# Kernel optimization log

Measured on AMD Instinct MI355X. Metric: run time of the kernel, lower is better.

## Reference

```python
import jax, jax.numpy as jnp
import numpy as np


def setup_inputs() -> dict:
    key = jax.random.key(0)
    k1, k2, k3, k4 = jax.random.split(key, 4)
    E, A = 1024, 64
    embedded = jax.random.normal(k1, (4, 4096, E), dtype=jnp.float32)
    # nn.Linear(E, A, bias=False) weight has shape [A, E]; y = x @ W.T
    W_K = jax.random.normal(k2, (A, E), dtype=jnp.float32) * (E ** -0.5)
    W_Q = jax.random.normal(k3, (A, E), dtype=jnp.float32) * (E ** -0.5)
    W_V = jax.random.normal(k4, (A, E), dtype=jnp.float32) * (E ** -0.5)
    return {"embedded": embedded, "W_K": W_K, "W_Q": W_Q, "W_V": W_V}


def reference(embedded, W_K, W_Q, W_V):
    A = W_K.shape[0]
    K = jnp.einsum('bse,ae->bsa', embedded, W_K)
    Q = jnp.einsum('bse,ae->bsa', embedded, W_Q)
    V = jnp.einsum('bse,ae->bsa', embedded, W_V)
    scores = jnp.einsum('bqa,bka->bqk', Q, K) / jnp.sqrt(jnp.float32(A))
    S = K.shape[1]
    causal = jnp.tril(jnp.ones((S, S), dtype=bool))  # True = keep
    scores = jnp.where(causal[None, :, :], scores, -jnp.inf)
    attn = jax.nn.softmax(scores, axis=2)
    out = jnp.einsum('bqk,bka->bqa', attn, V)
    return jnp.round(out, decimals=4)
```

## Files before the change

### kernel.cpp

```cpp
#include <hip/hip_runtime.h>
#include <math.h>

#define B_DIM 4
#define S_DIM 4096
#define E_DIM 1024
#define A_DIM 64
#define M_TOT (B_DIM * S_DIM)

typedef __bf16 v8bf __attribute__((ext_vector_type(8)));
typedef __bf16 v4bf __attribute__((ext_vector_type(4)));
typedef float  v4f  __attribute__((ext_vector_type(4)));

__device__ __forceinline__ v4f mfma16(v8bf a, v8bf b, v4f c) {
    return __builtin_amdgcn_mfma_f32_16x16x32_bf16(a, b, c, 0, 0, 0);
}

__device__ __forceinline__ void lds_dma16(const void* g, void* l) {
    __builtin_amdgcn_global_load_lds(
        (const __attribute__((address_space(1))) unsigned int*)g,
        (__attribute__((address_space(3))) unsigned int*)l, 16, 0, 0);
}

__global__ __launch_bounds__(256) void wconv_kernel(
    const float* __restrict__ Wk, const float* __restrict__ Wq,
    const float* __restrict__ Wv, __bf16* __restrict__ Wb)
{
    const int i = blockIdx.x * 256 + threadIdx.x;
    const int w = i >> 14;
    const int off = (i & 16383) * 4;
    const float* s = ((w == 0) ? Wk : (w == 1) ? Wq : Wv) + off;
    float4 v = *(const float4*)s;
    v4bf o;
    o[0] = (__bf16)v.x; o[1] = (__bf16)v.y; o[2] = (__bf16)v.z; o[3] = (__bf16)v.w;
    *(v4bf*)(Wb + (size_t)w * 65536 + off) = o;
}

__global__ __launch_bounds__(256) void qkv_proj_mfma(
    const float* __restrict__ X,
    const __bf16* __restrict__ Wb,
    __bf16* __restrict__ Kb,
    __bf16* __restrict__ Qb,
    __bf16* __restrict__ Vt)
{
    const int r0   = blockIdx.x * 32;
    const int w    = threadIdx.x >> 6;
    const int lane = threadIdx.x & 63;
    const int L    = lane & 15;
    const int quad = lane >> 4;
    const int cbase = w * 48;

    __shared__ __align__(16) char smem[9216 + 49152];
    __bf16* Xs = (__bf16*)smem;
    __bf16* Bs = (__bf16*)(smem + 9216);
    float (*Tv)[65] = (float(*)[65])smem;

    v4f acc[2][3];
#pragma unroll
    for (int mi = 0; mi < 2; ++mi)
#pragma unroll
        for (int nt = 0; nt < 3; ++nt) acc[mi][nt] = (v4f){0.f, 0.f, 0.f, 0.f};

    const int brow_l  = lane >> 3;
    const int bchunk  = lane & 7;
    const int bgchunk = bchunk ^ brow_l;
    auto stageB = [&](int kc, int buf) {
#pragma unroll
        for (int j = 0; j < 6; ++j) {
            const int rowbase = w * 48 + j * 8;
            const __bf16* g = Wb + (size_t)(rowbase + brow_l) * E_DIM
                              + kc * 64 + bgchunk * 8;
            lds_dma16(g, Bs + buf * 12288 + rowbase * 64);
        }
    };

    const int xrow_i = (lane >> 4);
    const int xcol   = (lane & 15) * 4;
    float4 xr[2];
    auto loadX = [&](int kc) {
#pragma unroll
        for (int i = 0; i < 2; ++i) {
            const int row = i * 16 + w * 4 + xrow_i;
            xr[i] = *(const float4*)(X + (size_t)(r0 + row) * E_DIM + kc * 64 + xcol);
        }
    };
    auto flushX = [&](int buf) {
#pragma unroll
        for (int i = 0; i < 2; ++i) {
            const int row = i * 16 + w * 4 + xrow_i;
            v4bf o;
            o[0] = (__bf16)xr[i].x; o[1] = (__bf16)xr[i].y;
            o[2] = (__bf16)xr[i].z; o[3] = (__bf16)xr[i].w;
            *(v4bf*)(Xs + buf * 2304 + row * 72 + xcol) = o;
        }
    };

    stageB(0, 0);
    loadX(0);
    flushX(0);
    __syncthreads();

#pragma unroll 1
    for (int kc = 0; kc < 16; ++kc) {
        const int cur = kc & 1;
        if (kc < 15) {
            stageB(kc + 1, cur ^ 1);
            loadX(kc + 1);
        }
        v8bf afr[2][2];
#pragma unroll
        for (int mi = 0; mi < 2; ++mi)
#pragma unroll
            for (int ka = 0; ka < 2; ++ka)
                afr[mi][ka] = *(const v8bf*)(Xs + cur * 2304 +
                                (mi * 16 + L) * 72 + ka * 32 + quad * 8);
        v8bf bfr[3][2];
#pragma unroll
        for (int nt = 0; nt < 3; ++nt)
#pragma unroll
            for (int ka = 0; ka < 2; ++ka) {
                const int R = cbase + nt * 16 + L;
                const int slot = (ka * 4 + quad) ^ (R & 7);
                bfr[nt][ka] = *(const v8bf*)(Bs + cur * 12288 + R * 64 + slot * 8);
            }
#pragma unroll
        for (int mi = 0; mi < 2; ++mi)
#pragma unroll
            for (int nt = 0; nt < 3; ++nt)
#pragma unroll
                for (int ka = 0; ka < 2; ++ka)
                    acc[mi][nt] = mfma16(afr[mi][ka], bfr[nt][ka], acc[mi][nt]);

        if (kc < 15) flushX(cur ^ 1);
        __syncthreads();
    }

#pragma unroll
    for (int nt = 0; nt < 3; ++nt) {
        const int c0 = cbase + nt * 16;
        if (c0 < 64) {
#pragma unroll
            for (int mi = 0; mi < 2; ++mi)
#pragma unroll
                for (int r = 0; r < 4; ++r)
                    Kb[(size_t)(r0 + mi * 16 + quad * 4 + r) * A_DIM + c0 + L] =
                        (__bf16)acc[mi][nt][r];
        } else if (c0 < 128) {
#pragma unroll
            for (int mi = 0; mi < 2; ++mi)
#pragma unroll
                for (int r = 0; r < 4; ++r)
                    Qb[(size_t)(r0 + mi * 16 + quad * 4 + r) * A_DIM + (c0 - 64) + L] =
                        (__bf16)(acc[mi][nt][r] * 0.125f);
        } else {
#pragma unroll
            for (int mi = 0; mi < 2; ++mi)
#pragma unroll
                for (int r = 0; r < 4; ++r)
                    Tv[mi * 16 + quad * 4 + r][(c0 - 128) + L] = acc[mi][nt][r];
        }
    }
    __syncthreads();

    {
        const int batch = r0 >> 12;
        const int s0    = r0 & 4095;
        const int a     = threadIdx.x >> 2;
        const int part  = threadIdx.x & 3;
        __bf16* vrow = Vt + (size_t)(batch * 64 + a) * S_DIM + s0 + part * 8;
        v8bf pk;
#pragma unroll
        for (int j = 0; j < 8; ++j)
            pk[j] = (__bf16)Tv[part * 8 + j][a];
        *(v8bf*)vrow = pk;
    }
}

__global__ __launch_bounds__(512, 2) void attn_fused(
    const __bf16* __restrict__ Qb,
    const __bf16* __restrict__ Kb,
    const __bf16* __restrict__ Vt,
    float* __restrict__ out)
{
    const int b  = blockIdx.y;
    const int qt = blockIdx.x;

    const int w    = threadIdx.x >> 6;
    const int lane = threadIdx.x & 63;
    const int L    = lane & 15;
    const int quad = lane >> 4;

    __shared__ __align__(16) char smem[73728];
    __bf16 (*Pt)[64][72]   = (__bf16(*)[64][72])smem;
    float*  red_l          = (float*)smem;
    float (*red_o)[64][65] = (float(*)[64][65])(smem + 2048);
    float*  invs           = (float*)(smem + 2048 + 66560);

    v8bf qf[4][2];
#pragma unroll
    for (int ni = 0; ni < 4; ++ni)
#pragma unroll
        for (int ka = 0; ka < 2; ++ka)
            qf[ni][ka] = *(const v8bf*)(Qb +
                (size_t)(b * S_DIM + qt * 64 + ni * 16 + L) * A_DIM + ka * 32 + quad * 8);

    v4f acc_o[4][4];
#pragma unroll
    for (int i = 0; i < 4; ++i)
#pragma unroll
        for (int j = 0; j < 4; ++j) acc_o[i][j] = (v4f){0.f, 0.f, 0.f, 0.f};
    float lrun[4] = {0.f, 0.f, 0.f, 0.f};

    for (int kt = w; kt <= qt; kt += 8) {
        v8bf kf[4][2];
#pragma unroll
        for (int mi = 0; mi < 4; ++mi)
#pragma unroll
            for (int ka = 0; ka < 2; ++ka)
                kf[mi][ka] = *(const v8bf*)(Kb +
                    (size_t)(b * S_DIM + kt * 64 + mi * 16 + L) * A_DIM + ka * 32 + quad * 8);
        v8bf vf[4][2];
#pragma unroll
        for (int ma = 0; ma < 4; ++ma)
#pragma unroll
            for (int ki = 0; ki < 2; ++ki)
                vf[ma][ki] = *(const v8bf*)(Vt +
                    (size_t)(b * 64 + ma * 16 + L) * S_DIM + kt * 64 + ki * 32 + quad * 8);

        const bool diag = (kt == qt);

#pragma unroll
        for (int ni = 0; ni < 4; ++ni) {
            v4f s[4];
#pragma unroll
            for (int mi = 0; mi < 4; ++mi) s[mi] = (v4f){0.f, 0.f, 0.f, 0.f};
#pragma unroll
            for (int mi = 0; mi < 4; ++mi)
#pragma unroll
                for (int ka = 0; ka < 2; ++ka)
                    s[mi] = mfma16(kf[mi][ka], qf[ni][ka], s[mi]);

            float rs = 0.f;
#pragma unroll
            for (int mi = 0; mi < 4; ++mi) {
                v4bf p4;
#pragma unroll
                for (int r = 0; r < 4; ++r) {
                    const bool masked = diag && (mi * 16 + quad * 4 + r > ni * 16 + L);
                    const float p = masked ? 0.f : __expf(s[mi][r]);
                    rs += p;
                    p4[r] = (__bf16)p;
                }
                *(v4bf*)&Pt[w][ni * 16 + L][mi * 16 + quad * 4] = p4;
            }
            lrun[ni] += rs;
        }

        v8bf pf[4][2];
#pragma unroll
        for (int ni = 0; ni < 4; ++ni)
#pragma unroll
            for (int ki = 0; ki < 2; ++ki)
                pf[ni][ki] = *(const v8bf*)&Pt[w][ni * 16 + L][ki * 32 + quad * 8];
#pragma unroll
        for (int ma = 0; ma < 4; ++ma)
#pragma unroll
            for (int ni = 0; ni < 4; ++ni)
#pragma unroll
                for (int ki = 0; ki < 2; ++ki)
                    acc_o[ma][ni] = mfma16(vf[ma][ki], pf[ni][ki], acc_o[ma][ni]);
    }

#pragma unroll
    for (int ni = 0; ni < 4; ++ni) {
        lrun[ni] += __shfl_xor(lrun[ni], 16, 64);
        lrun[ni] += __shfl_xor(lrun[ni], 32, 64);
    }

    __syncthreads();

    if (quad == 0) {
#pragma unroll
        for (int ni = 0; ni < 4; ++ni)
            red_l[w * 64 + ni * 16 + L] = lrun[ni];
    }
    if (w >= 4) {
#pragma unroll
        for (int ma = 0; ma < 4; ++ma)
#pragma unroll
            for (int ni = 0; ni < 4; ++ni)
#pragma unroll
                for (int r = 0; r < 4; ++r)
                    red_o[w - 4][ma * 16 + quad * 4 + r][ni * 16 + L] = acc_o[ma][ni][r];
    }
    __syncthreads();

    if (w < 4) {
#pragma unroll
        for (int ma = 0; ma < 4; ++ma)
#pragma unroll
            for (int ni = 0; ni < 4; ++ni)
#pragma unroll
                for (int r = 0; r < 4; ++r)
                    acc_o[ma][ni][r] += red_o[w][ma * 16 + quad * 4 + r][ni * 16 + L];
    } else if (w == 4) {
        float d = 0.f;
#pragma unroll
        for (int c = 0; c < 8; ++c) d += red_l[c * 64 + lane];
        invs[lane] = 1.0f / d;
    }
    __syncthreads();

    if (w < 4) {
#pragma unroll
        for (int ma = 0; ma < 4; ++ma)
#pragma unroll
            for (int ni = 0; ni < 4; ++ni)
#pragma unroll
                for (int r = 0; r < 4; ++r)
                    red_o[w][ma * 16 + quad * 4 + r][ni * 16 + L] = acc_o[ma][ni][r];
    }
    __syncthreads();

    {
        const int q  = threadIdx.x >> 3;
        const int ac = (threadIdx.x & 7) << 3;
        const float sc = invs[q];
        float* dst = out + (size_t)(b * S_DIM + qt * 64 + q) * A_DIM + ac;
#pragma unroll
        for (int i4 = 0; i4 < 2; ++i4) {
            float vv[4];
#pragma unroll
            for (int j = 0; j < 4; ++j) {
                const int a = ac + i4 * 4 + j;
                vv[j] = sc * (red_o[0][a][q] + red_o[1][a][q]
                            + red_o[2][a][q] + red_o[3][a][q]);
            }
            *(float4*)(dst + i4 * 4) = make_float4(vv[0], vv[1], vv[2], vv[3]);
        }
    }
}

extern "C" void kernel_launch(void* const* d_in, const int* in_sizes, int n_in,
                              void* d_out, int out_size, void* d_ws, size_t ws_size,
                              hipStream_t stream)
{
    const float* X  = (const float*)d_in[0];
    const float* Wk = (const float*)d_in[1];
    const float* Wq = (const float*)d_in[2];
    const float* Wv = (const float*)d_in[3];
    float* out = (float*)d_out;

    __bf16* Kb = (__bf16*)d_ws;
    __bf16* Qb = Kb + (size_t)M_TOT * A_DIM;
    __bf16* Vt = Qb + (size_t)M_TOT * A_DIM;
    __bf16* Wb = Vt + (size_t)M_TOT * A_DIM;

    wconv_kernel<<<192, 256, 0, stream>>>(Wk, Wq, Wv, Wb);

    qkv_proj_mfma<<<512, 256, 0, stream>>>(X, Wb, Kb, Qb, Vt);

    dim3 g2(64, B_DIM), b2(512);
    attn_fused<<<g2, b2, 0, stream>>>(Qb, Kb, Vt, out);
}
```

Before: 147.1 us.

## Split QKV projection across K/Q/V blocks with XCD-aware block mapping

The projection kernel now launches three times as many blocks, each computing only one of K, Q or V for a 32-row tile. This cuts per-block LDS and register use so more blocks fit per CU. The block index is remapped so the three blocks sharing an X tile land on the same XCD, which should let the repeated X reads hit in its L2. The trade-off is that X is read and converted to bf16 three times instead of once.

```diff
diff --git a/kernel.cpp b/kernel.cpp
--- a/kernel.cpp
+++ b/kernel.cpp
@@ -35,41 +35,44 @@
     *(v4bf*)(Wb + (size_t)w * 65536 + off) = o;
 }
 
-__global__ __launch_bounds__(256) void qkv_proj_mfma(
+__global__ __launch_bounds__(256, 6) void qkv_proj_mfma(
     const float* __restrict__ X,
     const __bf16* __restrict__ Wb,
     __bf16* __restrict__ Kb,
     __bf16* __restrict__ Qb,
     __bf16* __restrict__ Vt)
 {
-    const int r0   = blockIdx.x * 32;
+    const int bid = blockIdx.x;
+    const int xcd = bid & 7;
+    const int jj0 = bid >> 3;
+    const int cls = jj0 % 3;
+    const int m   = (jj0 / 3) * 8 + xcd;
+    const int r0  = m * 32;
+
     const int w    = threadIdx.x >> 6;
     const int lane = threadIdx.x & 63;
     const int L    = lane & 15;
     const int quad = lane >> 4;
-    const int cbase = w * 48;
-
-    __shared__ __align__(16) char smem[9216 + 49152];
+    const int cbase = w * 16;
+
+    __shared__ __align__(16) char smem[9216 + 16384];
     __bf16* Xs = (__bf16*)smem;
     __bf16* Bs = (__bf16*)(smem + 9216);
     float (*Tv)[65] = (float(*)[65])smem;
 
-    v4f acc[2][3];
-#pragma unroll
-    for (int mi = 0; mi < 2; ++mi)
-#pragma unroll
-        for (int nt = 0; nt < 3; ++nt) acc[mi][nt] = (v4f){0.f, 0.f, 0.f, 0.f};
+    v4f acc[2];
+    acc[0] = (v4f){0.f, 0.f, 0.f, 0.f};
+    acc[1] = (v4f){0.f, 0.f, 0.f, 0.f};
 
     const int brow_l  = lane >> 3;
-    const int bchunk  = lane & 7;
-    const int bgchunk = bchunk ^ brow_l;
+    const int bgchunk = (lane & 7) ^ brow_l;
     auto stageB = [&](int kc, int buf) {
 #pragma unroll
-        for (int j = 0; j < 6; ++j) {
-            const int rowbase = w * 48 + j * 8;
-            const __bf16* g = Wb + (size_t)(rowbase + brow_l) * E_DIM
+        for (int j = 0; j < 2; ++j) {
+            const int rowbase = w * 16 + j * 8;
+            const __bf16* g = Wb + (size_t)(cls * 64 + rowbase + brow_l) * E_DIM
                               + kc * 64 + bgchunk * 8;
-            lds_dma16(g, Bs + buf * 12288 + rowbase * 64);
+            lds_dma16(g, Bs + buf * 4096 + rowbase * 64);
         }
     };
 
@@ -113,55 +116,44 @@
             for (int ka = 0; ka < 2; ++ka)
                 afr[mi][ka] = *(const v8bf*)(Xs + cur * 2304 +
                                 (mi * 16 + L) * 72 + ka * 32 + quad * 8);
-        v8bf bfr[3][2];
-#pragma unroll
-        for (int nt = 0; nt < 3; ++nt)
-#pragma unroll
-            for (int ka = 0; ka < 2; ++ka) {
-                const int R = cbase + nt * 16 + L;
-                const int slot = (ka * 4 + quad) ^ (R & 7);
-                bfr[nt][ka] = *(const v8bf*)(Bs + cur * 12288 + R * 64 + slot * 8);
-            }
-#pragma unroll
-        for (int mi = 0; mi < 2; ++mi)
-#pragma unroll
-            for (int nt = 0; nt < 3; ++nt)
-#pragma unroll
-                for (int ka = 0; ka < 2; ++ka)
-                    acc[mi][nt] = mfma16(afr[mi][ka], bfr[nt][ka], acc[mi][nt]);
+        v8bf bfr[2];
+#pragma unroll
+        for (int ka = 0; ka < 2; ++ka) {
+            const int R = cbase + L;
+            const int slot = (ka * 4 + quad) ^ (R & 7);
+            bfr[ka] = *(const v8bf*)(Bs + cur * 4096 + R * 64 + slot * 8);
+        }
+#pragma unroll
+        for (int mi = 0; mi < 2; ++mi)
+#pragma unroll
+            for (int ka = 0; ka < 2; ++ka)
+                acc[mi] = mfma16(afr[mi][ka], bfr[ka], acc[mi]);
 
         if (kc < 15) flushX(cur ^ 1);
         __syncthreads();
     }
 
-#pragma unroll
-    for (int nt = 0; nt < 3; ++nt) {
-        const int c0 = cbase + nt * 16;
-        if (c0 < 64) {
-#pragma unroll
-            for (int mi = 0; mi < 2; ++mi)
-#pragma unroll
-                for (int r = 0; r < 4; ++r)
-                    Kb[(size_t)(r0 + mi * 16 + quad * 4 + r) * A_DIM + c0 + L] =
-                        (__bf16)acc[mi][nt][r];
-        } else if (c0 < 128) {
-#pragma unroll
-            for (int mi = 0; mi < 2; ++mi)
-#pragma unroll
-                for (int r = 0; r < 4; ++r)
-                    Qb[(size_t)(r0 + mi * 16 + quad * 4 + r) * A_DIM + (c0 - 64) + L] =
-                        (__bf16)(acc[mi][nt][r] * 0.125f);
-        } else {
-#pragma unroll
-            for (int mi = 0; mi < 2; ++mi)
-#pragma unroll
-                for (int r = 0; r < 4; ++r)
-                    Tv[mi * 16 + quad * 4 + r][(c0 - 128) + L] = acc[mi][nt][r];
-        }
-    }
-    __syncthreads();
-
-    {
+    if (cls == 0) {
+#pragma unroll
+        for (int mi = 0; mi < 2; ++mi)
+#pragma unroll
+            for (int r = 0; r < 4; ++r)
+                Kb[(size_t)(r0 + mi * 16 + quad * 4 + r) * A_DIM + cbase + L] =
+                    (__bf16)acc[mi][r];
+    } else if (cls == 1) {
+#pragma unroll
+        for (int mi = 0; mi < 2; ++mi)
+#pragma unroll
+            for (int r = 0; r < 4; ++r)
+                Qb[(size_t)(r0 + mi * 16 + quad * 4 + r) * A_DIM + cbase + L] =
+                    (__bf16)(acc[mi][r] * 0.125f);
+    } else {
+#pragma unroll
+        for (int mi = 0; mi < 2; ++mi)
+#pragma unroll
+            for (int r = 0; r < 4; ++r)
+                Tv[mi * 16 + quad * 4 + r][cbase + L] = acc[mi][r];
+        __syncthreads();
         const int batch = r0 >> 12;
         const int s0    = r0 & 4095;
         const int a     = threadIdx.x >> 2;
@@ -357,7 +349,7 @@
 
     wconv_kernel<<<192, 256, 0, stream>>>(Wk, Wq, Wv, Wb);
 
-    qkv_proj_mfma<<<512, 256, 0, stream>>>(X, Wb, Kb, Qb, Vt);
+    qkv_proj_mfma<<<1536, 256, 0, stream>>>(X, Wb, Kb, Qb, Vt);
 
     dim3 g2(64, B_DIM), b2(512);
     attn_fused<<<g2, b2, 0, stream>>>(Qb, Kb, Vt, out);
```

New measurement: 150.0 us. No clear change (+2.0%).

## Load QKV projection operands directly from global memory, dropping LDS staging

Applied to the files above, without the earlier changes.

The QKV projection kernel no longer stages X and the bf16 weights through double-buffered shared memory with DMA and barriers. Each wave now reads its MFMA fragments straight from global memory and converts X to bf16 in registers. This removes the LDS traffic and per-iteration __syncthreads and shrinks shared memory to the transpose buffer, which could raise occupancy. In exchange, X rows are re-read by all four waves and each weight fragment by every block, leaning on cache, and the loads are less coalesced.

```diff
diff --git a/kernel.cpp b/kernel.cpp
--- a/kernel.cpp
+++ b/kernel.cpp
@@ -13,12 +13,6 @@
 
 __device__ __forceinline__ v4f mfma16(v8bf a, v8bf b, v4f c) {
     return __builtin_amdgcn_mfma_f32_16x16x32_bf16(a, b, c, 0, 0, 0);
-}
-
-__device__ __forceinline__ void lds_dma16(const void* g, void* l) {
-    __builtin_amdgcn_global_load_lds(
-        (const __attribute__((address_space(1))) unsigned int*)g,
-        (__attribute__((address_space(3))) unsigned int*)l, 16, 0, 0);
 }
 
 __global__ __launch_bounds__(256) void wconv_kernel(
@@ -49,10 +43,7 @@
     const int quad = lane >> 4;
     const int cbase = w * 48;
 
-    __shared__ __align__(16) char smem[9216 + 49152];
-    __bf16* Xs = (__bf16*)smem;
-    __bf16* Bs = (__bf16*)(smem + 9216);
-    float (*Tv)[65] = (float(*)[65])smem;
+    __shared__ __align__(16) float Tv[32][65];
 
     v4f acc[2][3];
 #pragma unroll
@@ -60,78 +51,32 @@
 #pragma unroll
         for (int nt = 0; nt < 3; ++nt) acc[mi][nt] = (v4f){0.f, 0.f, 0.f, 0.f};
 
-    const int brow_l  = lane >> 3;
-    const int bchunk  = lane & 7;
-    const int bgchunk = bchunk ^ brow_l;
-    auto stageB = [&](int kc, int buf) {
-#pragma unroll
-        for (int j = 0; j < 6; ++j) {
-            const int rowbase = w * 48 + j * 8;
-            const __bf16* g = Wb + (size_t)(rowbase + brow_l) * E_DIM
-                              + kc * 64 + bgchunk * 8;
-            lds_dma16(g, Bs + buf * 12288 + rowbase * 64);
+    const float* xbase0 = X + (size_t)(r0 + L) * E_DIM + quad * 8;
+    const float* xbase1 = X + (size_t)(r0 + 16 + L) * E_DIM + quad * 8;
+    const __bf16* wb0 = Wb + (size_t)(cbase + L) * E_DIM + quad * 8;
+
+#pragma unroll 2
+    for (int c = 0; c < 32; ++c) {
+        v8bf afr[2];
+#pragma unroll
+        for (int mi = 0; mi < 2; ++mi) {
+            const float* xp = (mi ? xbase1 : xbase0) + c * 32;
+            float4 x0 = *(const float4*)xp;
+            float4 x1 = *(const float4*)(xp + 4);
+            afr[mi][0] = (__bf16)x0.x; afr[mi][1] = (__bf16)x0.y;
+            afr[mi][2] = (__bf16)x0.z; afr[mi][3] = (__bf16)x0.w;
+            afr[mi][4] = (__bf16)x1.x; afr[mi][5] = (__bf16)x1.y;
+            afr[mi][6] = (__bf16)x1.z; afr[mi][7] = (__bf16)x1.w;
         }
-    };
-
-    const int xrow_i = (lane >> 4);
-    const int xcol   = (lane & 15) * 4;
-    float4 xr[2];
-    auto loadX = [&](int kc) {
-#pragma unroll
-        for (int i = 0; i < 2; ++i) {
-            const int row = i * 16 + w * 4 + xrow_i;
-            xr[i] = *(const float4*)(X + (size_t)(r0 + row) * E_DIM + kc * 64 + xcol);
-        }
-    };
-    auto flushX = [&](int buf) {
-#pragma unroll
-        for (int i = 0; i < 2; ++i) {
-            const int row = i * 16 + w * 4 + xrow_i;
-            v4bf o;
-            o[0] = (__bf16)xr[i].x; o[1] = (__bf16)xr[i].y;
-            o[2] = (__bf16)xr[i].z; o[3] = (__bf16)xr[i].w;
-            *(v4bf*)(Xs + buf * 2304 + row * 72 + xcol) = o;
-        }
-    };
-
-    stageB(0, 0);
-    loadX(0);
-    flushX(0);
-    __syncthreads();
-
-#pragma unroll 1
-    for (int kc = 0; kc < 16; ++kc) {
-        const int cur = kc & 1;
-        if (kc < 15) {
-            stageB(kc + 1, cur ^ 1);
-            loadX(kc + 1);
-        }
-        v8bf afr[2][2];
+        v8bf bfr[3];
+#pragma unroll
+        for (int nt = 0; nt < 3; ++nt)
+            bfr[nt] = *(const v8bf*)(wb0 + (size_t)nt * 16 * E_DIM + c * 32);
 #pragma unroll
         for (int mi = 0; mi < 2; ++mi)
 #pragma unroll
-            for (int ka = 0; ka < 2; ++ka)
-                afr[mi][ka] = *(const v8bf*)(Xs + cur * 2304 +
-                                (mi * 16 + L) * 72 + ka * 32 + quad * 8);
-        v8bf bfr[3][2];
-#pragma unroll
-        for (int nt = 0; nt < 3; ++nt)
-#pragma unroll
-            for (int ka = 0; ka < 2; ++ka) {
-                const int R = cbase + nt * 16 + L;
-                const int slot = (ka * 4 + quad) ^ (R & 7);
-                bfr[nt][ka] = *(const v8bf*)(Bs + cur * 12288 + R * 64 + slot * 8);
-            }
-#pragma unroll
-        for (int mi = 0; mi < 2; ++mi)
-#pragma unroll
             for (int nt = 0; nt < 3; ++nt)
-#pragma unroll
-                for (int ka = 0; ka < 2; ++ka)
-                    acc[mi][nt] = mfma16(afr[mi][ka], bfr[nt][ka], acc[mi][nt]);
-
-        if (kc < 15) flushX(cur ^ 1);
-        __syncthreads();
+                acc[mi][nt] = mfma16(afr[mi], bfr[nt], acc[mi][nt]);
     }
 
 #pragma unroll
```

Measured after the change: 173.0 us. 1.18x slower.
